# Kernel optimization log

Measured on AMD Instinct MI355X. Metric: run time of the kernel, lower is better.

Reference implementation:

```python
import jax, jax.numpy as jnp
import numpy as np

N = 100000        # nodes
E = 1600000       # edges (avg degree 16)
HID = 64          # hidden_dim
IN = 64           # input_dim
H = 4             # GAT heads
C = HID // H      # per-head channels (hidden//4)
LN_EPS = 1e-5
NEG_SLOPE = 0.2   # PyG GATConv default


def setup_inputs() -> dict:
    key = jax.random.key(0)
    ks = jax.random.split(key, 12)

    def nrm(k, shape, fan_in):
        return jax.random.normal(k, shape, jnp.float32) / np.sqrt(fan_in).astype(np.float32)

    x = jax.random.normal(ks[0], (N, IN), jnp.float32)
    edge_index = jax.random.randint(ks[1], (2, E), 0, N, jnp.int32)
    return {
        "x": x,
        "edge_index": edge_index,
        "emb_W": nrm(ks[2], (HID, IN), IN),
        "emb_b": jnp.zeros((HID,), jnp.float32),
        "e8_W": nrm(ks[3], (3, HID, HID), HID),
        "gat_W": nrm(ks[4], (3, HID, H * C), HID),
        "att_src": nrm(ks[5], (3, H, C), C),
        "att_dst": nrm(ks[6], (3, H, C), C),
        "gat_b": jnp.zeros((3, HID), jnp.float32),
        "fus_W": nrm(ks[7], (3, HID, 2 * HID), 2 * HID),
        "fus_b": jnp.zeros((3, HID), jnp.float32),
        "ln_g": jnp.ones((3, HID), jnp.float32),
        "ln_b": jnp.zeros((3, HID), jnp.float32),
        "r_W1": nrm(ks[8], (HID // 2, HID), HID),
        "r_b1": jnp.zeros((HID // 2,), jnp.float32),
        "r_W2": nrm(ks[9], (1, HID // 2), HID // 2),
        "r_b2": jnp.zeros((1,), jnp.float32),
    }


def _forward(x, edge_index, emb_W, emb_b, e8_W, gat_W, att_src, att_dst, gat_b,
             fus_W, fus_b, ln_g, ln_b, r_W1, r_b1, r_W2, r_b2):
    n = x.shape[0]
    row, col = edge_index[0], edge_index[1]

    # --- E8 symmetric normalization (depends only on graph; constant across layers) ---
    deg = jax.ops.segment_sum(jnp.ones_like(col, dtype=jnp.float32), col, num_segments=n)
    dinv = jnp.where(deg > 0, deg ** -0.5, 0.0)           # inf -> 0 as in torch code
    vals = dinv[row] * dinv[col]                           # [E]

    # --- GAT self-loops (PyG GATConv add_self_loops=True) ---
    loop = jnp.arange(n, dtype=row.dtype)
    src = jnp.concatenate([row, loop])                     # [E+N]
    dst = jnp.concatenate([col, loop])                     # [E+N]

    h = x @ emb_W.T + emb_b                                # embedding: [N, HID]

    for i in range(3):  # fixed 3 structurally-distinct blocks
        res = h
        # E8: sparse adj matmul then linear (no bias)
        x_e8 = jax.ops.segment_sum(vals[:, None] * h[col], row, num_segments=n) @ e8_W[i].T

        # GATConv (heads=4, concat)
        g = (h @ gat_W[i]).reshape(n, H, C)                # [N,H,C]
        a_s = (g * att_src[i]).sum(-1)                     # [N,H]
        a_d = (g * att_dst[i]).sum(-1)                     # [N,H]
        e = jax.nn.leaky_relu(a_s[src] + a_d[dst], NEG_SLOPE)   # [E+N,H]
        m = jax.lax.stop_gradient(jax.ops.segment_max(e, dst, num_segments=n))
        ee = jnp.exp(e - m[dst])
        s = jax.ops.segment_sum(ee, dst, num_segments=n)   # [N,H], >0 (self-loops)
        alpha = ee / s[dst]                                # per-dst softmax
        x_gat = jax.ops.segment_sum(alpha[:, :, None] * g[src], dst, num_segments=n)
        x_gat = x_gat.reshape(n, H * C) + gat_b[i]

        # fusion + residual + LayerNorm + ReLU (dropout is identity in eval)
        h = jnp.concatenate([x_e8, x_gat], axis=-1) @ fus_W[i].T + fus_b[i]
        h = h + res
        mu = h.mean(-1, keepdims=True)
        var = ((h - mu) ** 2).mean(-1, keepdims=True)
        h = (h - mu) * jax.lax.rsqrt(var + LN_EPS) * ln_g[i] + ln_b[i]
        h = jax.nn.relu(h)

    h1 = jax.nn.relu(h @ r_W1.T + r_b1)                    # [N, HID//2]
    return jax.nn.sigmoid(h1 @ r_W2.T + r_b2)              # [N, 1]


def reference(x, edge_index, emb_W, emb_b, e8_W, gat_W, att_src, att_dst, gat_b,
              fus_W, fus_b, ln_g, ln_b, r_W1, r_b1, r_W2, r_b2):
    return _forward(x, edge_index, emb_W, emb_b, e8_W, gat_W, att_src, att_dst, gat_b,
                    fus_W, fus_b, ln_g, ln_b, r_W1, r_b1, r_W2, r_b2)
```

## Files before the change

kernel.cpp:

```cpp
#include <hip/hip_runtime.h>
#include <hip/hip_bf16.h>
#include <hip/hip_fp16.h>

typedef __hip_bfloat16 bf16;
typedef unsigned short ushort_t;
typedef unsigned short us8 __attribute__((ext_vector_type(8)));
typedef _Float16 half8 __attribute__((ext_vector_type(8)));
typedef float f32x4 __attribute__((ext_vector_type(4)));

#define NEG 0.2f
#define LNEPS 1e-5f
#define BWD 512

__device__ __forceinline__ int plaus(unsigned int lo){
    lo &= 0x7FFFu;
    if (lo == 0) return 1;
    unsigned int ex = (lo >> 7) & 0xFF;
    return (ex >= 100 && ex <= 140) ? 1 : 0;
}

__device__ __forceinline__ float decode_slot(const ushort_t* s, long long i, int fl){
    long long base = i << fl;
    unsigned int hi = s[base + fl];
    unsigned int lo = s[base];
    unsigned int bits = (hi << 16) | (lo * (unsigned int)fl);
    return __uint_as_float(bits);
}

__device__ __forceinline__ unsigned encf(float f){
    int b = __float_as_int(f);
    return (b >= 0) ? ((unsigned)b | 0x80000000u) : (unsigned)(~b);
}
__device__ __forceinline__ float decf(unsigned k){
    return (k & 0x80000000u) ? __uint_as_float(k & 0x7FFFFFFFu)
                             : __uint_as_float(~k);
}

#define P_TOTAL 56577
#define CONV_BLKS 222
__global__ __launch_bounds__(256) void k_init(const void* p0, const void* p1, const void* p2,
        const void* p3, const void* p4, const void* p5, const void* p6, const void* p7,
        const void* p8, const void* p9, const void* p10, const void* p11, const void* p12,
        const void* p13, const void* p14, const void* xs,
        const int* __restrict__ row, const int* __restrict__ col, int E, int NBK,
        int* flags, float* P, int* bcnt, unsigned* mxsu){
    __shared__ int lh[512];
    int t = threadIdx.x;
    if (blockIdx.x >= CONV_BLKS){
        int hb = blockIdx.x - CONV_BLKS;
        for (int i = t; i < 2*NBK; i += 256) lh[i] = 0;
        __syncthreads();
        for (long long e = (long long)hb*256 + t; e < E; e += (long long)256*256){
            atomicAdd(&lh[row[e] >> 9], 1);
            atomicAdd(&lh[NBK + (col[e] >> 9)], 1);
        }
        __syncthreads();
        for (int i = t; i < 2*NBK; i += 256){
            int v = lh[i];
            if (v) atomicAdd(&bcnt[i], v);
        }
        return;
    }
    if (blockIdx.x == 0){
        if (t < 9){
            const void* dt[9] = {xs, p0, p2, p3, p4, p5, p7, p11, p13};
            const ushort_t* w = (const ushort_t*)dt[t];
            int all_bf = 1;
            for (int i = 0; i < 16; i++) all_bf &= plaus((unsigned int)w[i]);
            flags[t] = all_bf ? 0 : 1;
        } else if (t == 9){
            const ushort_t* w = (const ushort_t*)p9;
            flags[9] = (w[0] == 0x3F80u) ? 0 : 1;
        }
        if (t < 32) mxsu[t] = 0u;
    }
    int idx = blockIdx.x*256 + t;
    if (idx >= P_TOTAL) return;
    const int sizes[15] = {4096,64,12288,12288,192,192,192,24576,192,192,192,2048,32,32,1};
    const int fidx[15]  = {1,  -1,  2,    3,    4,  5,  -1, 6,    -1, 9,  -1, 7,   -1,8, -1};
    const void* ptrs[15] = {p0,p1,p2,p3,p4,p5,p6,p7,p8,p9,p10,p11,p12,p13,p14};
    int s = 0, base = 0;
    while (idx - base >= sizes[s]){ base += sizes[s]; s++; }
    int li = idx - base;
    int fi = fidx[s];
    int fl = 0;
    if (fi == 9){
        const ushort_t* w = (const ushort_t*)ptrs[s];
        fl = (w[0] == 0x3F80u) ? 0 : 1;
    } else if (fi >= 0){
        const ushort_t* w = (const ushort_t*)ptrs[s];
        int all_bf = 1;
        for (int i = 0; i < 16; i++) all_bf &= plaus((unsigned int)w[i]);
        fl = all_bf ? 0 : 1;
    }
    P[idx] = decode_slot((const ushort_t*)ptrs[s], li, fl);
}

#define PRW_B0 (3*8192)
#define PRW_B1 (PRW_B0 + 192)
#define PRW_B2 (PRW_B1 + 3*5120)
__global__ __launch_bounds__(256) void kb_scanprew(const int* __restrict__ bcnt,
        int* __restrict__ bptr_r, int* __restrict__ bptr_c,
        int* __restrict__ bcur_r, int* __restrict__ bcur_c, int NBK, int E,
        const float* __restrict__ fus_W, const float* __restrict__ e8_W,
        const float* __restrict__ gat_b, const float* __restrict__ fus_b,
        const float* __restrict__ gat_W, const float* __restrict__ att_src,
        const float* __restrict__ att_dst,
        _Float16* __restrict__ Bfrag, float* __restrict__ b2c, _Float16* __restrict__ Bg){
    __shared__ int sh[256];
    int t = threadIdx.x;
    if (blockIdx.x < 2){
        int side = blockIdx.x;
        const int* c = bcnt + side*NBK;
        int* bp = side ? bptr_c : bptr_r;
        int* bc = side ? bcur_c : bcur_r;
        int v = (t < NBK) ? c[t] : 0;
        sh[t] = v; __syncthreads();
        for (int off = 1; off < 256; off <<= 1){
            int add = (t >= off) ? sh[t-off] : 0;
// ... 179 lines not shown
            #pragma unroll
            for (int j = 0; j < 8; j++){
                A0[j] = (_Float16)__uint_as_float((unsigned)r0[j] << 16);
                A1[j] = (_Float16)__uint_as_float((unsigned)r1[j] << 16);
            }
        } else {
            const f32x4* xf = (const f32x4*)xs;
            f32x4 f0 = xf[(size_t)anode*16 + q*2];
            f32x4 f1 = xf[(size_t)anode*16 + q*2 + 1];
            f32x4 f2 = xf[(size_t)anode*16 + 8 + q*2];
            f32x4 f3 = xf[(size_t)anode*16 + 8 + q*2 + 1];
            #pragma unroll
            for (int j = 0; j < 4; j++){
                A0[j] = (_Float16)f0[j]; A0[4+j] = (_Float16)f1[j];
                A1[j] = (_Float16)f2[j]; A1[4+j] = (_Float16)f3[j];
            }
        }
        f32x4 acc[4];
        #pragma unroll
        for (int t = 0; t < 4; t++){
            f32x4 z = {0.f, 0.f, 0.f, 0.f};
            z = __builtin_amdgcn_mfma_f32_16x16x32_f16(A0, Be[t][0], z, 0, 0, 0);
            z = __builtin_amdgcn_mfma_f32_16x16x32_f16(A1, Be[t][1], z, 0, 0, 0);
            acc[t] = z;
        }
        #pragma unroll
        for (int r = 0; r < 4; r++){
            int node = nb + q*4 + r;
            int nd2 = q*4 + r;
            #pragma unroll
            for (int t = 0; t < 4; t++){
                float out = acc[t][r] + bj[t];
                int byte = nd2*128 + (t*16 + c)*2;
                byte ^= (nd2 & 7) << 4;
                *(_Float16*)((char*)tb + byte) = (_Float16)out;
                if (node < N){
                    h16[(size_t)node*64 + t*16 + c] = __float2half(out);
                    ht16[(size_t)node*64 + t*16 + c] = __float2half(dinv[node]*out);
                }
            }
        }
        int b0 = (c*128 + 16*q) ^ ((c & 7) << 4);
        int b1 = (c*128 + 64 + 16*q) ^ ((c & 7) << 4);
        half8 A0g = *(half8*)((char*)tb + b0);
        half8 A1g = *(half8*)((char*)tb + b1);
        f32x4 gacc[5];
        #pragma unroll
        for (int t = 0; t < 5; t++){
            f32x4 z = {0.f, 0.f, 0.f, 0.f};
            z = __builtin_amdgcn_mfma_f32_16x16x32_f16(A0g, Bg[t][0], z, 0, 0, 0);
            z = __builtin_amdgcn_mfma_f32_16x16x32_f16(A1g, Bg[t][1], z, 0, 0, 0);
            gacc[t] = z;
        }
        #pragma unroll
        for (int r = 0; r < 4; r++) lmax = fmaxf(lmax, gacc[4][r]);
        #pragma unroll
        for (int r = 0; r < 4; r++){
            int node = nb + q*4 + r;
            if (node < N){
                #pragma unroll
                for (int t = 0; t < 4; t++)
                    G16[(size_t)node*64 + t*16 + c] = __float2half(gacc[t][r]);
                if (c < 8){
                    int hx = c >> 1;
                    if (c & 1) a_d[node*4+hx] = gacc[4][r];
                    else       a_s[node*4+hx] = gacc[4][r];
                }
            }
        }
    }
    lmax = fmaxf(lmax, __shfl_xor(lmax, 16));
    lmax = fmaxf(lmax, __shfl_xor(lmax, 32));
    if (lane < 8) redm[wv][lane] = lmax;
    __syncthreads();
    if (threadIdx.x < 8){
        float m = fmaxf(fmaxf(redm[0][threadIdx.x], redm[1][threadIdx.x]),
                        fmaxf(redm[2][threadIdx.x], redm[3][threadIdx.x]));
        int hx = threadIdx.x >> 1;
        int ix = (threadIdx.x & 1) ? 4 + hx : hx;
        atomicMax((unsigned*)mxs + ix, encf(m));
    }
}

__device__ __forceinline__ float leaky(float t){ return t > 0.f ? t : NEG*t; }

__global__ __launch_bounds__(256) void k_gather(const __half* __restrict__ ht16,
        const __half* __restrict__ G16,
        const float* __restrict__ a_s, const float* __restrict__ a_d,
        const float* __restrict__ mxs, const float* __restrict__ dinv,
        const int* __restrict__ row_ptr, const int* __restrict__ re_col,
        const int* __restrict__ col_ptr, const int* __restrict__ ce_row,
        __half* __restrict__ Aj16, __half* __restrict__ xg16, int N){
    int lane = threadIdx.x & 63;
    int grp  = lane >> 3;
    int sub  = lane & 7;
    int hh   = sub >> 1;
    int wid  = (blockIdx.x*blockDim.x + threadIdx.x) >> 6;
    int v    = wid*8 + grp;
    if (v >= N) return;
    const us8* htb = (const us8*)ht16;
    const us8* gb  = (const us8*)G16;
    const unsigned* mu = (const unsigned*)mxs;
    float sh = leaky(decf(mu[hh]) + decf(mu[4+hh]));
    int rs = row_ptr[v], re = row_ptr[v+1];
    float a0[8] = {0,0,0,0,0,0,0,0}, a1[8] = {0,0,0,0,0,0,0,0};
    float a2[8] = {0,0,0,0,0,0,0,0}, a3[8] = {0,0,0,0,0,0,0,0};
    int i = rs;
    for (; i + 3 < re; i += 4){
        us8 q0 = htb[(size_t)re_col[i]*8 + sub];
        us8 q1 = htb[(size_t)re_col[i+1]*8 + sub];
        us8 q2 = htb[(size_t)re_col[i+2]*8 + sub];
        us8 q3 = htb[(size_t)re_col[i+3]*8 + sub];
        #pragma unroll
        for (int j = 0; j < 8; j++){
            a0[j] += __half2float(__ushort_as_half(q0[j]));
            a1[j] += __half2float(__ushort_as_half(q1[j]));
            a2[j] += __half2float(__ushort_as_half(q2[j]));
            a3[j] += __half2float(__ushort_as_half(q3[j]));
        }
    }
    for (; i < re; i++){
        us8 q0 = htb[(size_t)re_col[i]*8 + sub];
        #pragma unroll
        for (int j = 0; j < 8; j++) a0[j] += __half2float(__ushort_as_half(q0[j]));
    }
    float dv = dinv[v];
    us8 pa;
    #pragma unroll
    for (int j = 0; j < 8; j++)
        pa[j] = __half_as_ushort(__float2half(dv*((a0[j]+a1[j]) + (a2[j]+a3[j]))));
    ((us8*)Aj16)[(size_t)v*8 + sub] = pa;
    float adv = a_d[v*4+hh];
    float eesl = __expf(leaky(a_s[v*4+hh] + adv) - sh);
    float s0 = eesl, s1 = 0.f, s2 = 0.f, s3 = 0.f;
    {
        us8 g0 = gb[(size_t)v*8 + sub];
        #pragma unroll
        for (int j = 0; j < 8; j++){
            a0[j] = eesl * __half2float(__ushort_as_half(g0[j]));
            a1[j] = 0.f; a2[j] = 0.f; a3[j] = 0.f;
        }
    }
    int cs = col_ptr[v], ce = col_ptr[v+1];
    i = cs;
    for (; i + 3 < ce; i += 4){
        int r0 = ce_row[i], r1 = ce_row[i+1], r2 = ce_row[i+2], r3 = ce_row[i+3];
        float e0 = __expf(leaky(a_s[r0*4+hh] + adv) - sh);
        float e1 = __expf(leaky(a_s[r1*4+hh] + adv) - sh);
        float e2 = __expf(leaky(a_s[r2*4+hh] + adv) - sh);
        float e3 = __expf(leaky(a_s[r3*4+hh] + adv) - sh);
        us8 q0 = gb[(size_t)r0*8 + sub];
        us8 q1 = gb[(size_t)r1*8 + sub];
        us8 q2 = gb[(size_t)r2*8 + sub];
        us8 q3 = gb[(size_t)r3*8 + sub];
        #pragma unroll
        for (int j = 0; j < 8; j++){
            a0[j] += e0 * __half2float(__ushort_as_half(q0[j]));
            a1[j] += e1 * __half2float(__ushort_as_half(q1[j]));
            a2[j] += e2 * __half2float(__ushort_as_half(q2[j]));
            a3[j] += e3 * __half2float(__ushort_as_half(q3[j]));
        }
        s0 += e0; s1 += e1; s2 += e2; s3 += e3;
    }
    for (; i < ce; i++){
        int r0 = ce_row[i];
        float e0 = __expf(leaky(a_s[r0*4+hh] + adv) - sh);
        us8 q0 = gb[(size_t)r0*8 + sub];
        #pragma unroll
        for (int j = 0; j < 8; j++) a0[j] += e0 * __half2float(__ushort_as_half(q0[j]));
        s0 += e0;
    }
    float inv = 1.f/((s0+s1)+(s2+s3));
    us8 px;
    #pragma unroll
    for (int j = 0; j < 8; j++)
        px[j] = __half_as_ushort(__float2half(((a0[j]+a1[j]) + (a2[j]+a3[j]))*inv));
    ((us8*)xg16)[(size_t)v*8 + sub] = px;
}

__global__ __launch_bounds__(256) void k_fuse_g(
        const __half* __restrict__ Aj16, const __half* __restrict__ xg16,
        const float* __restrict__ dinv, __half* __restrict__ h16,
        __half* __restrict__ ht16,
        const _Float16* __restrict__ Bfrag, const float* __restrict__ b2c,
        const float* __restrict__ ln_g, const float* __restrict__ ln_b,
        const _Float16* __restrict__ Bgn, __half* __restrict__ G16,
        float* __restrict__ a_s, float* __restrict__ a_d,
        float* __restrict__ mxs_next, int N){
    __shared__ float redm[4][8];
    __shared__ _Float16 tbuf[4][1024];
    int lane = threadIdx.x & 63;
    int wv = threadIdx.x >> 6;
    int q = lane >> 4, c = lane & 15;
    _Float16* tb = tbuf[wv];
    half8 B[4][4];
    const half8* Bp = (const half8*)Bfrag;
    #pragma unroll
    for (int t = 0; t < 4; t++)
        #pragma unroll
        for (int kk = 0; kk < 4; kk++)
            B[t][kk] = Bp[(t*4+kk)*64 + lane];
    half8 Bg[5][2];
    const half8* Bgp = (const half8*)Bgn;
    #pragma unroll
    for (int t = 0; t < 5; t++)
        #pragma unroll
        for (int kk = 0; kk < 2; kk++)
            Bg[t][kk] = Bgp[(t*2+kk)*64 + lane];
    float bj[4], lg[4], lb[4];
    #pragma unroll
    for (int t = 0; t < 4; t++){
        int n = t*16 + c;
        bj[t] = b2c[n]; lg[t] = ln_g[n]; lb[t] = ln_b[n];
    }
    float lmax = -1e30f;
    int tiles = (N + 15) >> 4;
    int wid = (blockIdx.x*blockDim.x + threadIdx.x) >> 6;
    int nw  = (gridDim.x*blockDim.x) >> 6;
    for (int tile = wid; tile < tiles; tile += nw){
        int nb = tile << 4;
        int anode = nb + c; if (anode >= N) anode = N - 1;
        const half8* ap = (const half8*)(Aj16 + (size_t)anode*64);
        const half8* xp = (const half8*)(xg16 + (size_t)anode*64);
        half8 A0 = ap[q];
        half8 A1 = ap[4 + q];
        half8 A2 = xp[q];
        half8 A3 = xp[4 + q];
        f32x4 acc[4];
        #pragma unroll
        for (int t = 0; t < 4; t++){
            f32x4 z = {0.f, 0.f, 0.f, 0.f};
            z = __builtin_amdgcn_mfma_f32_16x16x32_f16(A0, B[t][0], z, 0, 0, 0);
            z = __builtin_amdgcn_mfma_f32_16x16x32_f16(A1, B[t][1], z, 0, 0, 0);
            z = __builtin_amdgcn_mfma_f32_16x16x32_f16(A2, B[t][2], z, 0, 0, 0);
            z = __builtin_amdgcn_mfma_f32_16x16x32_f16(A3, B[t][3], z, 0, 0, 0);
            acc[t] = z;
        }
        float y[4][4];
        #pragma unroll
        for (int r = 0; r < 4; r++){
            int node = nb + q*4 + r;
            int nd = node < N ? node : N - 1;
            #pragma unroll
            for (int t = 0; t < 4; t++)
                y[t][r] = acc[t][r] + bj[t]
                        + __half2float(h16[(size_t)nd*64 + t*16 + c]);
        }
        #pragma unroll
        for (int r = 0; r < 4; r++){
            int node = nb + q*4 + r;
            float s = (y[0][r] + y[1][r]) + (y[2][r] + y[3][r]);
            #pragma unroll
            for (int o = 1; o < 16; o <<= 1) s += __shfl_xor(s, o);
            float mu = s * (1.f/64.f);
            float d0 = y[0][r]-mu, d1 = y[1][r]-mu, d2 = y[2][r]-mu, d3 = y[3][r]-mu;
            float var = (d0*d0 + d1*d1) + (d2*d2 + d3*d3);
            #pragma unroll
            for (int o = 1; o < 16; o <<= 1) var += __shfl_xor(var, o);
            var *= (1.f/64.f);
            float rstd = rsqrtf(var + LNEPS);
            int nd2 = q*4 + r;
            #pragma unroll
            for (int t = 0; t < 4; t++){
                float out = (y[t][r]-mu)*rstd*lg[t] + lb[t];
                out = out > 0.f ? out : 0.f;
                int byte = nd2*128 + (t*16 + c)*2;
                byte ^= (nd2 & 7) << 4;
                *(_Float16*)((char*)tb + byte) = (_Float16)out;
                if (node < N){
                    h16[(size_t)node*64 + t*16 + c] = __float2half(out);
                    ht16[(size_t)node*64 + t*16 + c] = __float2half(dinv[node]*out);
                }
            }
        }
        int b0 = (c*128 + 16*q) ^ ((c & 7) << 4);
        int b1 = (c*128 + 64 + 16*q) ^ ((c & 7) << 4);
        half8 A0g = *(half8*)((char*)tb + b0);
        half8 A1g = *(half8*)((char*)tb + b1);
        f32x4 gacc[5];
        #pragma unroll
        for (int t = 0; t < 5; t++){
            f32x4 z = {0.f, 0.f, 0.f, 0.f};
            z = __builtin_amdgcn_mfma_f32_16x16x32_f16(A0g, Bg[t][0], z, 0, 0, 0);
            z = __builtin_amdgcn_mfma_f32_16x16x32_f16(A1g, Bg[t][1], z, 0, 0, 0);
            gacc[t] = z;
        }
        #pragma unroll
        for (int r = 0; r < 4; r++) lmax = fmaxf(lmax, gacc[4][r]);
        #pragma unroll
        for (int r = 0; r < 4; r++){
            int node = nb + q*4 + r;
            if (node < N){
                #pragma unroll
                for (int t = 0; t < 4; t++)
                    G16[(size_t)node*64 + t*16 + c] = __float2half(gacc[t][r]);
                if (c < 8){
                    int hx = c >> 1;
                    if (c & 1) a_d[node*4+hx] = gacc[4][r];
                    else       a_s[node*4+hx] = gacc[4][r];
                }
            }
        }
    }
    lmax = fmaxf(lmax, __shfl_xor(lmax, 16));
    lmax = fmaxf(lmax, __shfl_xor(lmax, 32));
    if (lane < 8) redm[wv][lane] = lmax;
    __syncthreads();
    if (threadIdx.x < 8){
        float m = fmaxf(fmaxf(redm[0][threadIdx.x], redm[1][threadIdx.x]),
                        fmaxf(redm[2][threadIdx.x], redm[3][threadIdx.x]));
        int hx = threadIdx.x >> 1;
        int ix = (threadIdx.x & 1) ? 4 + hx : hx;
        atomicMax((unsigned*)mxs_next + ix, encf(m));
    }
}

__global__ __launch_bounds__(256) void k_fuse_ro(
        const __half* __restrict__ Aj16, const __half* __restrict__ xg16,
        const __half* __restrict__ h16,
        const _Float16* __restrict__ Bfrag, const float* __restrict__ b2c,
        const float* __restrict__ ln_g, const float* __restrict__ ln_b,
        const float* __restrict__ rW1, const float* __restrict__ rb1,
        const float* __restrict__ rW2, const float* __restrict__ rb2,
        float* __restrict__ out, int N){
    __shared__ _Float16 tbuf[4][1024];
    int lane = threadIdx.x & 63;
    int wv = threadIdx.x >> 6;
    int q = lane >> 4, c = lane & 15;
    _Float16* tb = tbuf[wv];
    half8 B[4][4];
    const half8* Bp = (const half8*)Bfrag;
    #pragma unroll
    for (int t = 0; t < 4; t++)
        #pragma unroll
        for (int kk = 0; kk < 4; kk++)
            B[t][kk] = Bp[(t*4+kk)*64 + lane];
    half8 B1r[2][2];
    #pragma unroll
    for (int t = 0; t < 2; t++){
        #pragma unroll
        for (int kk = 0; kk < 2; kk++){
            half8 v;
            #pragma unroll
            for (int j = 0; j < 8; j++)
                v[j] = (_Float16)rW1[(t*16 + c)*64 + kk*32 + q*8 + j];
            B1r[t][kk] = v;
        }
    }
    float bj[4], lg[4], lb[4];
    #pragma unroll
    for (int t = 0; t < 4; t++){
        int n = t*16 + c;
        bj[t] = b2c[n]; lg[t] = ln_g[n]; lb[t] = ln_b[n];
    }
    float b1v[2] = {rb1[c], rb1[16 + c]};
    float w2a = rW2[c], w2b = rW2[16 + c];
    float b2v = rb2[0];
    int tiles = (N + 15) >> 4;
    int wid = (blockIdx.x*blockDim.x + threadIdx.x) >> 6;
    int nw  = (gridDim.x*blockDim.x) >> 6;
    for (int tile = wid; tile < tiles; tile += nw){
        int nb = tile << 4;
        int anode = nb + c; if (anode >= N) anode = N - 1;
        const half8* ap = (const half8*)(Aj16 + (size_t)anode*64);
        const half8* xp = (const half8*)(xg16 + (size_t)anode*64);
        half8 A0 = ap[q];
        half8 A1 = ap[4 + q];
        half8 A2 = xp[q];
        half8 A3 = xp[4 + q];
        f32x4 acc[4];
        #pragma unroll
        for (int t = 0; t < 4; t++){
            f32x4 z = {0.f, 0.f, 0.f, 0.f};
            z = __builtin_amdgcn_mfma_f32_16x16x32_f16(A0, B[t][0], z, 0, 0, 0);
            z = __builtin_amdgcn_mfma_f32_16x16x32_f16(A1, B[t][1], z, 0, 0, 0);
            z = __builtin_amdgcn_mfma_f32_16x16x32_f16(A2, B[t][2], z, 0, 0, 0);
            z = __builtin_amdgcn_mfma_f32_16x16x32_f16(A3, B[t][3], z, 0, 0, 0);
            acc[t] = z;
        }
        float y[4][4];
        #pragma unroll
        for (int r = 0; r < 4; r++){
            int node = nb + q*4 + r;
            int nd = node < N ? node : N - 1;
            #pragma unroll
            for (int t = 0; t < 4; t++)
                y[t][r] = acc[t][r] + bj[t]
                        + __half2float(h16[(size_t)nd*64 + t*16 + c]);
        }
        #pragma unroll
        for (int r = 0; r < 4; r++){
            float s = (y[0][r] + y[1][r]) + (y[2][r] + y[3][r]);
            #pragma unroll
            for (int o = 1; o < 16; o <<= 1) s += __shfl_xor(s, o);
            float mu = s * (1.f/64.f);
            float d0 = y[0][r]-mu, d1 = y[1][r]-mu, d2 = y[2][r]-mu, d3 = y[3][r]-mu;
            float var = (d0*d0 + d1*d1) + (d2*d2 + d3*d3);
            #pragma unroll
            for (int o = 1; o < 16; o <<= 1) var += __shfl_xor(var, o);
            var *= (1.f/64.f);
            float rstd = rsqrtf(var + LNEPS);
            int nd2 = q*4 + r;
            #pragma unroll
            for (int t = 0; t < 4; t++){
                float outv = (y[t][r]-mu)*rstd*lg[t] + lb[t];
                outv = outv > 0.f ? outv : 0.f;
                int byte = nd2*128 + (t*16 + c)*2;
                byte ^= (nd2 & 7) << 4;
                *(_Float16*)((char*)tb + byte) = (_Float16)outv;
            }
        }
        int b0 = (c*128 + 16*q) ^ ((c & 7) << 4);
        int b1 = (c*128 + 64 + 16*q) ^ ((c & 7) << 4);
        half8 A0g = *(half8*)((char*)tb + b0);
        half8 A1g = *(half8*)((char*)tb + b1);
        f32x4 racc[2];
        #pragma unroll
        for (int t = 0; t < 2; t++){
            f32x4 z = {0.f, 0.f, 0.f, 0.f};
            z = __builtin_amdgcn_mfma_f32_16x16x32_f16(A0g, B1r[t][0], z, 0, 0, 0);
            z = __builtin_amdgcn_mfma_f32_16x16x32_f16(A1g, B1r[t][1], z, 0, 0, 0);
            racc[t] = z;
        }
        #pragma unroll
        for (int r = 0; r < 4; r++){
            int node = nb + q*4 + r;
            float h1a = racc[0][r] + b1v[0]; h1a = h1a > 0.f ? h1a : 0.f;
            float h1b = racc[1][r] + b1v[1]; h1b = h1b > 0.f ? h1b : 0.f;
            float p = h1a*w2a + h1b*w2b;
            p += __shfl_xor(p, 1);
            p += __shfl_xor(p, 2);
            p += __shfl_xor(p, 4);
            p += __shfl_xor(p, 8);
            if (c == 0 && node < N){
                float z = p + b2v;
                out[node] = 1.f/(1.f + __expf(-z));
            }
        }
    }
}

extern "C" void kernel_launch(void* const* d_in, const int* in_sizes, int n_in,
                              void* d_out, int out_size, void* d_ws, size_t ws_size,
                              hipStream_t stream){
    const ushort_t* xs = (const ushort_t*)d_in[0];
    const int*      ei = (const int*)d_in[1];

    int N = in_sizes[0] / 64;
    int E = in_sizes[1] / 2;
    const int* row = ei;
    const int* col = ei + E;
    int NBK = (N + BWD - 1) / BWD;

    size_t mirF = (size_t)N*32;
    size_t stageF = (size_t)E;
    size_t aliasF = stageF > mirF ? stageF : mirF;

    float* f = (float*)d_ws;
    size_t o = 0;
    int*   flags = (int*)(f + o); o += 16;
    float* P     = f + o; o += P_TOTAL + 63;
    __half* h16  = (__half*)(f + o); o += mirF;
    __half* ht16 = (__half*)(f + o); o += mirF;
    __half* G16  = (__half*)(f + o); o += mirF;
    __half* Aj16 = (__half*)(f + o); size_t aoff = o; o += aliasF;
    __half* xg16 = (__half*)(f + o); size_t xoff = o; o += aliasF;
    unsigned* stage_r = (unsigned*)(f + aoff);
    unsigned* stage_c = (unsigned*)(f + xoff);
    float* a_s   = f + o; o += (size_t)N*4;
    float* a_d   = f + o; o += (size_t)N*4;
    float* mxs   = f + o; o += 32;
    float* dinv  = f + o; o += ((size_t)N + 15) & ~15ull;
    int* bcnt    = (int*)(f + o); o += 512;
    int* bptr_r  = (int*)(f + o); o += 512;
    int* bptr_c  = (int*)(f + o); o += 512;
    int* bcur_r  = (int*)(f + o); o += 512;
    int* bcur_c  = (int*)(f + o); o += 512;
    int* ptr_r   = (int*)(f + o); o += ((size_t)N + 16) & ~15ull;
    int* ptr_c   = (int*)(f + o); o += ((size_t)N + 16) & ~15ull;
    int* re_col  = (int*)(f + o); o += (size_t)E;
    int* ce_row  = (int*)(f + o); o += (size_t)E;
    float* b2c   = f + o; o += 3*64;
    _Float16* Bfrag = (_Float16*)(f + o); o += 3*4096;
    _Float16* Bg    = (_Float16*)(f + o); o += 3*2560;

    const float* emb_W   = P + 0;
    const float* emb_b   = P + 4096;
    const float* e8_W    = P + 4160;
    const float* gat_W   = P + 16448;
    const float* att_src = P + 28736;
    const float* att_dst = P + 28928;
    const float* gat_b   = P + 29120;
    const float* fus_W   = P + 29312;
    const float* fus_b   = P + 53888;
    const float* ln_g    = P + 54080;
    const float* ln_b    = P + 54272;
    const float* r_W1    = P + 54464;
    const float* r_b1    = P + 56512;
    const float* r_W2    = P + 56544;
    const float* r_b2    = P + 56576;

    hipMemsetAsync(bcnt, 0, 512*sizeof(int), stream);
    k_init<<<CONV_BLKS + 256, 256, 0, stream>>>(
        d_in[2],d_in[3],d_in[4],d_in[5],d_in[6],d_in[7],d_in[8],d_in[9],
        d_in[10],d_in[11],d_in[12],d_in[13],d_in[14],d_in[15],d_in[16],
        d_in[0], row, col, E, NBK, flags, P, bcnt, (unsigned*)mxs);

    int prwblk = (PRW_B2 + 255) / 256;
    kb_scanprew<<<2 + prwblk, 256, 0, stream>>>(bcnt, bptr_r, bptr_c, bcur_r, bcur_c,
                                                NBK, E, fus_W, e8_W, gat_b, fus_b,
                                                gat_W, att_src, att_dst, Bfrag, b2c, Bg);
    kb_bin<<<512, 1024, 0, stream>>>(row, col, bcur_r, bcur_c, stage_r, stage_c, NBK, E);
    kb_place<<<2*NBK, 1024, 0, stream>>>(stage_r, stage_c, bptr_r, bptr_c,
                                         ptr_r, ptr_c, re_col, ce_row, dinv, NBK, N, E);

    int tiles = (N + 15) / 16;
    int fgrid = (tiles + 7) / 8;
    int ggrid = (N + 31) / 32;
    k_embed_g<<<fgrid, 256, 0, stream>>>(xs, flags, emb_W, emb_b, dinv, Bg,
                                         h16, ht16, G16, a_s, a_d, mxs, N);
    for (int i = 0; i < 3; i++){
        k_gather<<<ggrid, 256, 0, stream>>>(ht16, G16, a_s, a_d, mxs + i*8, dinv,
                                            ptr_r, re_col, ptr_c, ce_row,
                                            Aj16, xg16, N);
        if (i < 2){
            k_fuse_g<<<fgrid, 256, 0, stream>>>(Aj16, xg16, dinv, h16, ht16,
                                                Bfrag + (size_t)i*8192, b2c + i*64,
                                                ln_g + i*64, ln_b + i*64,
                                                Bg + (size_t)(i+1)*5120, G16,
                                                a_s, a_d, mxs + (i+1)*8, N);
        } else {
            k_fuse_ro<<<fgrid, 256, 0, stream>>>(Aj16, xg16, h16,
                                                 Bfrag + (size_t)i*8192, b2c + i*64,
                                                 ln_g + i*64, ln_b + i*64,
                                                 r_W1, r_b1, r_W2, r_b2,
                                                 (float*)d_out, N);
        }
    }
}
```

Measured before the change: 635.8 us.

## Merge per-layer gather and fuse kernels into one persistent cooperative kernel

The six per-layer launches (gather, fuse, readout) are replaced by a single cooperative persistent kernel that loops over the three layers and uses grid-wide syncs between the gather and fuse phases. Weight fragments are now staged into shared memory per layer instead of being held in registers. This removes launch gaps and tail effects between the small kernels. In exchange it adds grid-sync overhead, caps the grid at occupancy-limited residency, and uses more LDS, which may reduce occupancy for the latency-bound gather phase.

```diff
diff --git a/kernel.cpp b/kernel.cpp
--- a/kernel.cpp
+++ b/kernel.cpp
@@ -1,6 +1,9 @@
 #include <hip/hip_runtime.h>
 #include <hip/hip_bf16.h>
 #include <hip/hip_fp16.h>
+#include <hip/hip_cooperative_groups.h>
+
+namespace cg = cooperative_groups;
 
 typedef __hip_bfloat16 bf16;
 typedef unsigned short ushort_t;
@@ -35,6 +38,8 @@
     return (k & 0x80000000u) ? __uint_as_float(k & 0x7FFFFFFFu)
                              : __uint_as_float(~k);
 }
+
+__device__ __forceinline__ float leaky(float t){ return t > 0.f ? t : NEG*t; }
 
 #define P_TOTAL 56577
 #define CONV_BLKS 222
@@ -380,361 +385,279 @@
     }
 }
 
-__device__ __forceinline__ float leaky(float t){ return t > 0.f ? t : NEG*t; }
-
-__global__ __launch_bounds__(256) void k_gather(const __half* __restrict__ ht16,
-        const __half* __restrict__ G16,
-        const float* __restrict__ a_s, const float* __restrict__ a_d,
-        const float* __restrict__ mxs, const float* __restrict__ dinv,
-        const int* __restrict__ row_ptr, const int* __restrict__ re_col,
-        const int* __restrict__ col_ptr, const int* __restrict__ ce_row,
-        __half* __restrict__ Aj16, __half* __restrict__ xg16, int N){
-    int lane = threadIdx.x & 63;
-    int grp  = lane >> 3;
-    int sub  = lane & 7;
-    int hh   = sub >> 1;
-    int wid  = (blockIdx.x*blockDim.x + threadIdx.x) >> 6;
-    int v    = wid*8 + grp;
-    if (v >= N) return;
+__global__ __launch_bounds__(256, 4) void k_layers(
+        __half* __restrict__ h16, __half* __restrict__ ht16, __half* __restrict__ G16,
+        float* __restrict__ a_s, float* __restrict__ a_d, float* __restrict__ mxs,
+        const float* __restrict__ dinv,
+        const int* __restrict__ ptr_r, const int* __restrict__ re_col,
+        const int* __restrict__ ptr_c, const int* __restrict__ ce_row,
+        const _Float16* __restrict__ BfragG, const float* __restrict__ b2cG,
+        const float* __restrict__ ln_gG, const float* __restrict__ ln_bG,
+        const _Float16* __restrict__ BgG,
+        const float* __restrict__ rW1, const float* __restrict__ rb1,
+        const float* __restrict__ rW2, const float* __restrict__ rb2,
+        __half* __restrict__ Aj16, __half* __restrict__ xg16,
+        float* __restrict__ out, int N){
+    cg::grid_group gridg = cg::this_grid();
+    __shared__ _Float16 Bsh[8192];
+    __shared__ _Float16 Bgsh[5120];
+    __shared__ _Float16 tbuf[4][1024];
+    __shared__ float redm[4][8];
+    int tid = threadIdx.x;
+    int lane = tid & 63, wv = tid >> 6;
+    int q = lane >> 4, c = lane & 15;
+    int grp = lane >> 3, sub = lane & 7, hh = sub >> 1;
+    _Float16* tb = tbuf[wv];
+    int wid0 = (blockIdx.x*256 + tid) >> 6;
+    int TW = (gridDim.x*256) >> 6;
+    const us8* gb  = (const us8*)G16;
     const us8* htb = (const us8*)ht16;
-    const us8* gb  = (const us8*)G16;
-    const unsigned* mu = (const unsigned*)mxs;
-    float sh = leaky(decf(mu[hh]) + decf(mu[4+hh]));
-    int rs = row_ptr[v], re = row_ptr[v+1];
-    float a0[8] = {0,0,0,0,0,0,0,0}, a1[8] = {0,0,0,0,0,0,0,0};
-    float a2[8] = {0,0,0,0,0,0,0,0}, a3[8] = {0,0,0,0,0,0,0,0};
-    int i = rs;
-    for (; i + 3 < re; i += 4){
-        us8 q0 = htb[(size_t)re_col[i]*8 + sub];
-        us8 q1 = htb[(size_t)re_col[i+1]*8 + sub];
-        us8 q2 = htb[(size_t)re_col[i+2]*8 + sub];
-        us8 q3 = htb[(size_t)re_col[i+3]*8 + sub];
-        #pragma unroll
-        for (int j = 0; j < 8; j++){
-            a0[j] += __half2float(__ushort_as_half(q0[j]));
-            a1[j] += __half2float(__ushort_as_half(q1[j]));
-            a2[j] += __half2float(__ushort_as_half(q2[j]));
-            a3[j] += __half2float(__ushort_as_half(q3[j]));
-        }
-    }
-    for (; i < re; i++){
-        us8 q0 = htb[(size_t)re_col[i]*8 + sub];
-        #pragma unroll
-        for (int j = 0; j < 8; j++) a0[j] += __half2float(__ushort_as_half(q0[j]));
-    }
-    float dv = dinv[v];
-    us8 pa;
-    #pragma unroll
-    for (int j = 0; j < 8; j++)
-        pa[j] = __half_as_ushort(__float2half(dv*((a0[j]+a1[j]) + (a2[j]+a3[j]))));
-    ((us8*)Aj16)[(size_t)v*8 + sub] = pa;
-    float adv = a_d[v*4+hh];
-    float eesl = __expf(leaky(a_s[v*4+hh] + adv) - sh);
-    float s0 = eesl, s1 = 0.f, s2 = 0.f, s3 = 0.f;
-    {
-        us8 g0 = gb[(size_t)v*8 + sub];
-        #pragma unroll
-        for (int j = 0; j < 8; j++){
-            a0[j] = eesl * __half2float(__ushort_as_half(g0[j]));
-            a1[j] = 0.f; a2[j] = 0.f; a3[j] = 0.f;
-        }
-    }
-    int cs = col_ptr[v], ce = col_ptr[v+1];
-    i = cs;
-    for (; i + 3 < ce; i += 4){
-        int r0 = ce_row[i], r1 = ce_row[i+1], r2 = ce_row[i+2], r3 = ce_row[i+3];
-        float e0 = __expf(leaky(a_s[r0*4+hh] + adv) - sh);
-        float e1 = __expf(leaky(a_s[r1*4+hh] + adv) - sh);
-        float e2 = __expf(leaky(a_s[r2*4+hh] + adv) - sh);
-        float e3 = __expf(leaky(a_s[r3*4+hh] + adv) - sh);
-        us8 q0 = gb[(size_t)r0*8 + sub];
-        us8 q1 = gb[(size_t)r1*8 + sub];
-        us8 q2 = gb[(size_t)r2*8 + sub];
-        us8 q3 = gb[(size_t)r3*8 + sub];
-        #pragma unroll
-        for (int j = 0; j < 8; j++){
-            a0[j] += e0 * __half2float(__ushort_as_half(q0[j]));
-            a1[j] += e1 * __half2float(__ushort_as_half(q1[j]));
-            a2[j] += e2 * __half2float(__ushort_as_half(q2[j]));
-            a3[j] += e3 * __half2float(__ushort_as_half(q3[j]));
-        }
-        s0 += e0; s1 += e1; s2 += e2; s3 += e3;
-    }
-    for (; i < ce; i++){
-        int r0 = ce_row[i];
-        float e0 = __expf(leaky(a_s[r0*4+hh] + adv) - sh);
-        us8 q0 = gb[(size_t)r0*8 + sub];
-        #pragma unroll
-        for (int j = 0; j < 8; j++) a0[j] += e0 * __half2float(__ushort_as_half(q0[j]));
-        s0 += e0;
-    }
-    float inv = 1.f/((s0+s1)+(s2+s3));
-    us8 px;
-    #pragma unroll
-    for (int j = 0; j < 8; j++)
-        px[j] = __half_as_ushort(__float2half(((a0[j]+a1[j]) + (a2[j]+a3[j]))*inv));
-    ((us8*)xg16)[(size_t)v*8 + sub] = px;
-}
-
-__global__ __launch_bounds__(256) void k_fuse_g(
-        const __half* __restrict__ Aj16, const __half* __restrict__ xg16,
-        const float* __restrict__ dinv, __half* __restrict__ h16,
-        __half* __restrict__ ht16,
-        const _Float16* __restrict__ Bfrag, const float* __restrict__ b2c,
-        const float* __restrict__ ln_g, const float* __restrict__ ln_b,
-        const _Float16* __restrict__ Bgn, __half* __restrict__ G16,
-        float* __restrict__ a_s, float* __restrict__ a_d,
-        float* __restrict__ mxs_next, int N){
-    __shared__ float redm[4][8];
-    __shared__ _Float16 tbuf[4][1024];
-    int lane = threadIdx.x & 63;
-    int wv = threadIdx.x >> 6;
-    int q = lane >> 4, c = lane & 15;
-    _Float16* tb = tbuf[wv];
-    half8 B[4][4];
-    const half8* Bp = (const half8*)Bfrag;
-    #pragma unroll
-    for (int t = 0; t < 4; t++)
-        #pragma unroll
-        for (int kk = 0; kk < 4; kk++)
-            B[t][kk] = Bp[(t*4+kk)*64 + lane];
-    half8 Bg[5][2];
-    const half8* Bgp = (const half8*)Bgn;
-    #pragma unroll
-    for (int t = 0; t < 5; t++)
-        #pragma unroll
-        for (int kk = 0; kk < 2; kk++)
-            Bg[t][kk] = Bgp[(t*2+kk)*64 + lane];
-    float bj[4], lg[4], lb[4];
-    #pragma unroll
-    for (int t = 0; t < 4; t++){
-        int n = t*16 + c;
-        bj[t] = b2c[n]; lg[t] = ln_g[n]; lb[t] = ln_b[n];
-    }
-    float lmax = -1e30f;
-    int tiles = (N + 15) >> 4;
-    int wid = (blockIdx.x*blockDim.x + threadIdx.x) >> 6;
-    int nw  = (gridDim.x*blockDim.x) >> 6;
-    for (int tile = wid; tile < tiles; tile += nw){
-        int nb = tile << 4;
-        int anode = nb + c; if (anode >= N) anode = N - 1;
-        const half8* ap = (const half8*)(Aj16 + (size_t)anode*64);
-        const half8* xp = (const half8*)(xg16 + (size_t)anode*64);
-        half8 A0 = ap[q];
-        half8 A1 = ap[4 + q];
-        half8 A2 = xp[q];
-        half8 A3 = xp[4 + q];
-        f32x4 acc[4];
+
+    for (int L = 0; L < 3; L++){
+        const unsigned* mup = (const unsigned*)mxs + L*8;
+        float shx = leaky(decf(mup[hh]) + decf(mup[4+hh]));
+        int NG = (N + 7) >> 3;
+        for (int w = wid0; w < NG; w += TW){
+            int v = w*8 + grp;
+            if (v < N){
+                int rs = ptr_r[v], re = ptr_r[v+1];
+                float a0[8] = {0,0,0,0,0,0,0,0}, a1[8] = {0,0,0,0,0,0,0,0};
+                float a2[8] = {0,0,0,0,0,0,0,0}, a3[8] = {0,0,0,0,0,0,0,0};
+                int i = rs;
+                for (; i + 3 < re; i += 4){
+                    us8 q0 = htb[(size_t)re_col[i]*8 + sub];
+                    us8 q1 = htb[(size_t)re_col[i+1]*8 + sub];
+                    us8 q2 = htb[(size_t)re_col[i+2]*8 + sub];
+                    us8 q3 = htb[(size_t)re_col[i+3]*8 + sub];
+                    #pragma unroll
+                    for (int j = 0; j < 8; j++){
+                        a0[j] += __half2float(__ushort_as_half(q0[j]));
+                        a1[j] += __half2float(__ushort_as_half(q1[j]));
+                        a2[j] += __half2float(__ushort_as_half(q2[j]));
+                        a3[j] += __half2float(__ushort_as_half(q3[j]));
+                    }
+                }
+                for (; i < re; i++){
+                    us8 q0 = htb[(size_t)re_col[i]*8 + sub];
+                    #pragma unroll
+                    for (int j = 0; j < 8; j++) a0[j] += __half2float(__ushort_as_half(q0[j]));
+                }
+                float dv = dinv[v];
+                us8 pa;
+                #pragma unroll
+                for (int j = 0; j < 8; j++)
+                    pa[j] = __half_as_ushort(__float2half(dv*((a0[j]+a1[j]) + (a2[j]+a3[j]))));
+                ((us8*)Aj16)[(size_t)v*8 + sub] = pa;
+                float adv = a_d[v*4+hh];
+                float eesl = __expf(leaky(a_s[v*4+hh] + adv) - shx);
+                float s0 = eesl, s1 = 0.f, s2 = 0.f, s3 = 0.f;
+                {
+                    us8 g0 = gb[(size_t)v*8 + sub];
+                    #pragma unroll
+                    for (int j = 0; j < 8; j++){
+                        a0[j] = eesl * __half2float(__ushort_as_half(g0[j]));
+                        a1[j] = 0.f; a2[j] = 0.f; a3[j] = 0.f;
+                    }
+                }
+                int cs = ptr_c[v], ce = ptr_c[v+1];
+                i = cs;
+                for (; i + 3 < ce; i += 4){
+                    int r0 = ce_row[i], r1 = ce_row[i+1], r2 = ce_row[i+2], r3 = ce_row[i+3];
+                    float e0 = __expf(leaky(a_s[r0*4+hh] + adv) - shx);
+                    float e1 = __expf(leaky(a_s[r1*4+hh] + adv) - shx);
+                    float e2 = __expf(leaky(a_s[r2*4+hh] + adv) - shx);
+                    float e3 = __expf(leaky(a_s[r3*4+hh] + adv) - shx);
+                    us8 q0 = gb[(size_t)r0*8 + sub];
+                    us8 q1 = gb[(size_t)r1*8 + sub];
+                    us8 q2 = gb[(size_t)r2*8 + sub];
+                    us8 q3 = gb[(size_t)r3*8 + sub];
+                    #pragma unroll
+                    for (int j = 0; j < 8; j++){
+                        a0[j] += e0 * __half2float(__ushort_as_half(q0[j]));
+                        a1[j] += e1 * __half2float(__ushort_as_half(q1[j]));
+                        a2[j] += e2 * __half2float(__ushort_as_half(q2[j]));
+                        a3[j] += e3 * __half2float(__ushort_as_half(q3[j]));
+                    }
+                    s0 += e0; s1 += e1; s2 += e2; s3 += e3;
+                }
+                for (; i < ce; i++){
+                    int r0 = ce_row[i];
+                    float e0 = __expf(leaky(a_s[r0*4+hh] + adv) - shx);
+                    us8 q0 = gb[(size_t)r0*8 + sub];
+                    #pragma unroll
+                    for (int j = 0; j < 8; j++) a0[j] += e0 * __half2float(__ushort_as_half(q0[j]));
+                    s0 += e0;
+                }
+                float inv = 1.f/((s0+s1)+(s2+s3));
+                us8 px;
+                #pragma unroll
+                for (int j = 0; j < 8; j++)
+                    px[j] = __half_as_ushort(__float2half(((a0[j]+a1[j]) + (a2[j]+a3[j]))*inv));
+                ((us8*)xg16)[(size_t)v*8 + sub] = px;
+            }
+        }
+        gridg.sync();
+
+        {
+            const half8* s = (const half8*)(BfragG + (size_t)L*8192);
+            half8* d = (half8*)Bsh;
+            for (int i = tid; i < 1024; i += 256) d[i] = s[i];
+        }
+        if (L < 2){
+            const half8* s = (const half8*)(BgG + (size_t)(L+1)*5120);
+            half8* d = (half8*)Bgsh;
+            for (int i = tid; i < 640; i += 256) d[i] = s[i];
+        } else {
+            for (int i = tid; i < 2048; i += 256){
+                int j = i & 7, ln = (i >> 3) & 63, kk = (i >> 9) & 1, tt = i >> 10;
+                int k = kk*32 + (ln >> 4)*8 + j;
+                int n = tt*16 + (ln & 15);
+                Bgsh[i] = (_Float16)rW1[n*64 + k];
+            }
+        }
+        __syncthreads();
+        const float* b2p = b2cG + L*64;
+        const float* lgp = ln_gG + L*64;
+        const float* lbp = ln_bG + L*64;
+        float bj[4], lg[4], lb[4];
         #pragma unroll
         for (int t = 0; t < 4; t++){
-            f32x4 z = {0.f, 0.f, 0.f, 0.f};
-            z = __builtin_amdgcn_mfma_f32_16x16x32_f16(A0, B[t][0], z, 0, 0, 0);
-            z = __builtin_amdgcn_mfma_f32_16x16x32_f16(A1, B[t][1], z, 0, 0, 0);
-            z = __builtin_amdgcn_mfma_f32_16x16x32_f16(A2, B[t][2], z, 0, 0, 0);
-            z = __builtin_amdgcn_mfma_f32_16x16x32_f16(A3, B[t][3], z, 0, 0, 0);
-            acc[t] = z;
-        }
-        float y[4][4];
-        #pragma unroll
-        for (int r = 0; r < 4; r++){
-            int node = nb + q*4 + r;
-            int nd = node < N ? node : N - 1;
-            #pragma unroll
-            for (int t = 0; t < 4; t++)
-                y[t][r] = acc[t][r] + bj[t]
-                        + __half2float(h16[(size_t)nd*64 + t*16 + c]);
-        }
-        #pragma unroll
-        for (int r = 0; r < 4; r++){
-            int node = nb + q*4 + r;
-            float s = (y[0][r] + y[1][r]) + (y[2][r] + y[3][r]);
-            #pragma unroll
-            for (int o = 1; o < 16; o <<= 1) s += __shfl_xor(s, o);
-            float mu = s * (1.f/64.f);
-            float d0 = y[0][r]-mu, d1 = y[1][r]-mu, d2 = y[2][r]-mu, d3 = y[3][r]-mu;
-            float var = (d0*d0 + d1*d1) + (d2*d2 + d3*d3);
-            #pragma unroll
-            for (int o = 1; o < 16; o <<= 1) var += __shfl_xor(var, o);
-            var *= (1.f/64.f);
-            float rstd = rsqrtf(var + LNEPS);
-            int nd2 = q*4 + r;
+            int n = t*16 + c;
+            bj[t] = b2p[n]; lg[t] = lgp[n]; lb[t] = lbp[n];
+        }
+        float b1v0 = 0.f, b1v1 = 0.f, w2a = 0.f, w2b = 0.f, b2v = 0.f;
+        if (L == 2){
+            b1v0 = rb1[c]; b1v1 = rb1[16 + c];
+            w2a = rW2[c];  w2b = rW2[16 + c];
+            b2v = rb2[0];
+        }
+        float lmax = -1e30f;
+        int tiles = (N + 15) >> 4;
+        for (int tile = wid0; tile < tiles; tile += TW){
+            int nb = tile << 4;
+            int anode = nb + c; if (anode >= N) anode = N - 1;
+            const half8* ap = (const half8*)(Aj16 + (size_t)anode*64);
+            const half8* xp = (const half8*)(xg16 + (size_t)anode*64);
+            half8 A0 = ap[q];
+            half8 A1 = ap[4 + q];
+            half8 A2 = xp[q];
+            half8 A3 = xp[4 + q];
+            f32x4 acc[4];
             #pragma unroll
             for (int t = 0; t < 4; t++){
-                float out = (y[t][r]-mu)*rstd*lg[t] + lb[t];
-                out = out > 0.f ? out : 0.f;
-                int byte = nd2*128 + (t*16 + c)*2;
-                byte ^= (nd2 & 7) << 4;
-                *(_Float16*)((char*)tb + byte) = (_Float16)out;
-                if (node < N){
-                    h16[(size_t)node*64 + t*16 + c] = __float2half(out);
-                    ht16[(size_t)node*64 + t*16 + c] = __float2half(dinv[node]*out);
-                }
-            }
-        }
-        int b0 = (c*128 + 16*q) ^ ((c & 7) << 4);
-        int b1 = (c*128 + 64 + 16*q) ^ ((c & 7) << 4);
-        half8 A0g = *(half8*)((char*)tb + b0);
-        half8 A1g = *(half8*)((char*)tb + b1);
-        f32x4 gacc[5];
-        #pragma unroll
-        for (int t = 0; t < 5; t++){
-            f32x4 z = {0.f, 0.f, 0.f, 0.f};
-            z = __builtin_amdgcn_mfma_f32_16x16x32_f16(A0g, Bg[t][0], z, 0, 0, 0);
-            z = __builtin_amdgcn_mfma_f32_16x16x32_f16(A1g, Bg[t][1], z, 0, 0, 0);
-            gacc[t] = z;
-        }
-        #pragma unroll
-        for (int r = 0; r < 4; r++) lmax = fmaxf(lmax, gacc[4][r]);
-        #pragma unroll
-        for (int r = 0; r < 4; r++){
-            int node = nb + q*4 + r;
-            if (node < N){
+                f32x4 z = {0.f, 0.f, 0.f, 0.f};
+                z = __builtin_amdgcn_mfma_f32_16x16x32_f16(A0, *(half8*)(Bsh + ((t*4+0)*64+lane)*8), z, 0, 0, 0);
+                z = __builtin_amdgcn_mfma_f32_16x16x32_f16(A1, *(half8*)(Bsh + ((t*4+1)*64+lane)*8), z, 0, 0, 0);
+                z = __builtin_amdgcn_mfma_f32_16x16x32_f16(A2, *(half8*)(Bsh + ((t*4+2)*64+lane)*8), z, 0, 0, 0);
+                z = __builtin_amdgcn_mfma_f32_16x16x32_f16(A3, *(half8*)(Bsh + ((t*4+3)*64+lane)*8), z, 0, 0, 0);
+                acc[t] = z;
+            }
+            float y[4][4];
+            #pragma unroll
+            for (int r = 0; r < 4; r++){
+                int node = nb + q*4 + r;
+                int nd = node < N ? node : N - 1;
                 #pragma unroll
                 for (int t = 0; t < 4; t++)
-                    G16[(size_t)node*64 + t*16 + c] = __float2half(gacc[t][r]);
-                if (c < 8){
-                    int hx = c >> 1;
-                    if (c & 1) a_d[node*4+hx] = gacc[4][r];
-                    else       a_s[node*4+hx] = gacc[4][r];
-                }
-            }
-        }
-    }
-    lmax = fmaxf(lmax, __shfl_xor(lmax, 16));
-    lmax = fmaxf(lmax, __shfl_xor(lmax, 32));
-    if (lane < 8) redm[wv][lane] = lmax;
-    __syncthreads();
-    if (threadIdx.x < 8){
-        float m = fmaxf(fmaxf(redm[0][threadIdx.x], redm[1][threadIdx.x]),
-                        fmaxf(redm[2][threadIdx.x], redm[3][threadIdx.x]));
-        int hx = threadIdx.x >> 1;
-        int ix = (threadIdx.x & 1) ? 4 + hx : hx;
-        atomicMax((unsigned*)mxs_next + ix, encf(m));
-    }
-}
-
-__global__ __launch_bounds__(256) void k_fuse_ro(
-        const __half* __restrict__ Aj16, const __half* __restrict__ xg16,
-        const __half* __restrict__ h16,
-        const _Float16* __restrict__ Bfrag, const float* __restrict__ b2c,
-        const float* __restrict__ ln_g, const float* __restrict__ ln_b,
-        const float* __restrict__ rW1, const float* __restrict__ rb1,
-        const float* __restrict__ rW2, const float* __restrict__ rb2,
-        float* __restrict__ out, int N){
-    __shared__ _Float16 tbuf[4][1024];
-    int lane = threadIdx.x & 63;
-    int wv = threadIdx.x >> 6;
-    int q = lane >> 4, c = lane & 15;
-    _Float16* tb = tbuf[wv];
-    half8 B[4][4];
-    const half8* Bp = (const half8*)Bfrag;
-    #pragma unroll
-    for (int t = 0; t < 4; t++)
-        #pragma unroll
-        for (int kk = 0; kk < 4; kk++)
-            B[t][kk] = Bp[(t*4+kk)*64 + lane];
-    half8 B1r[2][2];
-    #pragma unroll
-    for (int t = 0; t < 2; t++){
-        #pragma unroll
-        for (int kk = 0; kk < 2; kk++){
-            half8 v;
+                    y[t][r] = acc[t][r] + bj[t]
+                            + __half2float(h16[(size_t)nd*64 + t*16 + c]);
+            }
             #pragma unroll
-            for (int j = 0; j < 8; j++)
-                v[j] = (_Float16)rW1[(t*16 + c)*64 + kk*32 + q*8 + j];
-            B1r[t][kk] = v;
-        }
-    }
-    float bj[4], lg[4], lb[4];
-    #pragma unroll
-    for (int t = 0; t < 4; t++){
-        int n = t*16 + c;
-        bj[t] = b2c[n]; lg[t] = ln_g[n]; lb[t] = ln_b[n];
-    }
-    float b1v[2] = {rb1[c], rb1[16 + c]};
-    float w2a = rW2[c], w2b = rW2[16 + c];
-    float b2v = rb2[0];
-    int tiles = (N + 15) >> 4;
-    int wid = (blockIdx.x*blockDim.x + threadIdx.x) >> 6;
-    int nw  = (gridDim.x*blockDim.x) >> 6;
-    for (int tile = wid; tile < tiles; tile += nw){
-        int nb = tile << 4;
-        int anode = nb + c; if (anode >= N) anode = N - 1;
-        const half8* ap = (const half8*)(Aj16 + (size_t)anode*64);
-        const half8* xp = (const half8*)(xg16 + (size_t)anode*64);
-        half8 A0 = ap[q];
-        half8 A1 = ap[4 + q];
-        half8 A2 = xp[q];
-        half8 A3 = xp[4 + q];
-        f32x4 acc[4];
-        #pragma unroll
-        for (int t = 0; t < 4; t++){
-            f32x4 z = {0.f, 0.f, 0.f, 0.f};
-            z = __builtin_amdgcn_mfma_f32_16x16x32_f16(A0, B[t][0], z, 0, 0, 0);
-            z = __builtin_amdgcn_mfma_f32_16x16x32_f16(A1, B[t][1], z, 0, 0, 0);
-            z = __builtin_amdgcn_mfma_f32_16x16x32_f16(A2, B[t][2], z, 0, 0, 0);
-            z = __builtin_amdgcn_mfma_f32_16x16x32_f16(A3, B[t][3], z, 0, 0, 0);
-            acc[t] = z;
-        }
-        float y[4][4];
-        #pragma unroll
-        for (int r = 0; r < 4; r++){
-            int node = nb + q*4 + r;
-            int nd = node < N ? node : N - 1;
-            #pragma unroll
-            for (int t = 0; t < 4; t++)
-                y[t][r] = acc[t][r] + bj[t]
-                        + __half2float(h16[(size_t)nd*64 + t*16 + c]);
-        }
-        #pragma unroll
-        for (int r = 0; r < 4; r++){
-            float s = (y[0][r] + y[1][r]) + (y[2][r] + y[3][r]);
-            #pragma unroll
-            for (int o = 1; o < 16; o <<= 1) s += __shfl_xor(s, o);
-            float mu = s * (1.f/64.f);
-            float d0 = y[0][r]-mu, d1 = y[1][r]-mu, d2 = y[2][r]-mu, d3 = y[3][r]-mu;
-            float var = (d0*d0 + d1*d1) + (d2*d2 + d3*d3);
-            #pragma unroll
-            for (int o = 1; o < 16; o <<= 1) var += __shfl_xor(var, o);
-            var *= (1.f/64.f);
-            float rstd = rsqrtf(var + LNEPS);
-            int nd2 = q*4 + r;
-            #pragma unroll
-            for (int t = 0; t < 4; t++){
-                float outv = (y[t][r]-mu)*rstd*lg[t] + lb[t];
-                outv = outv > 0.f ? outv : 0.f;
-                int byte = nd2*128 + (t*16 + c)*2;
-                byte ^= (nd2 & 7) << 4;
-                *(_Float16*)((char*)tb + byte) = (_Float16)outv;
-            }
-        }
-        int b0 = (c*128 + 16*q) ^ ((c & 7) << 4);
-        int b1 = (c*128 + 64 + 16*q) ^ ((c & 7) << 4);
-        half8 A0g = *(half8*)((char*)tb + b0);
-        half8 A1g = *(half8*)((char*)tb + b1);
-        f32x4 racc[2];
-        #pragma unroll
-        for (int t = 0; t < 2; t++){
-            f32x4 z = {0.f, 0.f, 0.f, 0.f};
-            z = __builtin_amdgcn_mfma_f32_16x16x32_f16(A0g, B1r[t][0], z, 0, 0, 0);
-            z = __builtin_amdgcn_mfma_f32_16x16x32_f16(A1g, B1r[t][1], z, 0, 0, 0);
-            racc[t] = z;
-        }
-        #pragma unroll
-        for (int r = 0; r < 4; r++){
-            int node = nb + q*4 + r;
-            float h1a = racc[0][r] + b1v[0]; h1a = h1a > 0.f ? h1a : 0.f;
-            float h1b = racc[1][r] + b1v[1]; h1b = h1b > 0.f ? h1b : 0.f;
-            float p = h1a*w2a + h1b*w2b;
-            p += __shfl_xor(p, 1);
-            p += __shfl_xor(p, 2);
-            p += __shfl_xor(p, 4);
-            p += __shfl_xor(p, 8);
-            if (c == 0 && node < N){
-                float z = p + b2v;
-                out[node] = 1.f/(1.f + __expf(-z));
-            }
-        }
+            for (int r = 0; r < 4; r++){
+                int node = nb + q*4 + r;
+                float s = (y[0][r] + y[1][r]) + (y[2][r] + y[3][r]);
+                #pragma unroll
+                for (int o = 1; o < 16; o <<= 1) s += __shfl_xor(s, o);
+                float mu = s * (1.f/64.f);
+                float d0 = y[0][r]-mu, d1 = y[1][r]-mu, d2 = y[2][r]-mu, d3 = y[3][r]-mu;
+                float var = (d0*d0 + d1*d1) + (d2*d2 + d3*d3);
+                #pragma unroll
+                for (int o = 1; o < 16; o <<= 1) var += __shfl_xor(var, o);
+                var *= (1.f/64.f);
+                float rstd = rsqrtf(var + LNEPS);
+                int nd2 = q*4 + r;
+                #pragma unroll
+                for (int t = 0; t < 4; t++){
+                    float outv = (y[t][r]-mu)*rstd*lg[t] + lb[t];
+                    outv = outv > 0.f ? outv : 0.f;
+                    int byte = nd2*128 + (t*16 + c)*2;
+                    byte ^= (nd2 & 7) << 4;
+                    *(_Float16*)((char*)tb + byte) = (_Float16)outv;
+                    if (L < 2 && node < N){
+                        h16[(size_t)node*64 + t*16 + c] = __float2half(outv);
+                        ht16[(size_t)node*64 + t*16 + c] = __float2half(dinv[node]*outv);
+                    }
+                }
+            }
+            int bo0 = (c*128 + 16*q) ^ ((c & 7) << 4);
+            int bo1 = (c*128 + 64 + 16*q) ^ ((c & 7) << 4);
+            half8 A0g = *(half8*)((char*)tb + bo0);
+            half8 A1g = *(half8*)((char*)tb + bo1);
+            if (L < 2){
+                f32x4 gacc[5];
+                #pragma unroll
+                for (int t = 0; t < 5; t++){
+                    f32x4 z = {0.f, 0.f, 0.f, 0.f};
+                    z = __builtin_amdgcn_mfma_f32_16x16x32_f16(A0g, *(half8*)(Bgsh + ((t*2+0)*64+lane)*8), z, 0, 0, 0);
+                    z = __builtin_amdgcn_mfma_f32_16x16x32_f16(A1g, *(half8*)(Bgsh + ((t*2+1)*64+lane)*8), z, 0, 0, 0);
+                    gacc[t] = z;
+                }
+                #pragma unroll
+                for (int r = 0; r < 4; r++) lmax = fmaxf(lmax, gacc[4][r]);
+                #pragma unroll
+                for (int r = 0; r < 4; r++){
+                    int node = nb + q*4 + r;
+                    if (node < N){
+                        #pragma unroll
+                        for (int t = 0; t < 4; t++)
+                            G16[(size_t)node*64 + t*16 + c] = __float2half(gacc[t][r]);
+                        if (c < 8){
+                            int hx = c >> 1;
+                            if (c & 1) a_d[node*4+hx] = gacc[4][r];
+                            else       a_s[node*4+hx] = gacc[4][r];
+                        }
+                    }
+                }
+            } else {
+                f32x4 racc[2];
+                #pragma unroll
+                for (int t = 0; t < 2; t++){
+                    f32x4 z = {0.f, 0.f, 0.f, 0.f};
+                    z = __builtin_amdgcn_mfma_f32_16x16x32_f16(A0g, *(half8*)(Bgsh + ((t*2+0)*64+lane)*8), z, 0, 0, 0);
+                    z = __builtin_amdgcn_mfma_f32_16x16x32_f16(A1g, *(half8*)(Bgsh + ((t*2+1)*64+lane)*8), z, 0, 0, 0);
+                    racc[t] = z;
+                }
+                #pragma unroll
+                for (int r = 0; r < 4; r++){
+                    int node = nb + q*4 + r;
+                    float h1a = racc[0][r] + b1v0; h1a = h1a > 0.f ? h1a : 0.f;
+                    float h1b = racc[1][r] + b1v1; h1b = h1b > 0.f ? h1b : 0.f;
+                    float p = h1a*w2a + h1b*w2b;
+                    p += __shfl_xor(p, 1);
+                    p += __shfl_xor(p, 2);
+                    p += __shfl_xor(p, 4);
+                    p += __shfl_xor(p, 8);
+                    if (c == 0 && node < N){
+                        float z = p + b2v;
+                        out[node] = 1.f/(1.f + __expf(-z));
+                    }
+                }
+            }
+        }
+        if (L < 2){
+            lmax = fmaxf(lmax, __shfl_xor(lmax, 16));
+            lmax = fmaxf(lmax, __shfl_xor(lmax, 32));
+            if (lane < 8) redm[wv][lane] = lmax;
+            __syncthreads();
+            if (tid < 8){
+                float m = fmaxf(fmaxf(redm[0][tid], redm[1][tid]),
+                                fmaxf(redm[2][tid], redm[3][tid]));
+                int hx = tid >> 1;
+                int ix = (tid & 1) ? 4 + hx : hx;
+                atomicMax((unsigned*)mxs + (L+1)*8 + ix, encf(m));
+            }
+        }
+        gridg.sync();
     }
 }
 
@@ -814,25 +737,26 @@
 
     int tiles = (N + 15) / 16;
     int fgrid = (tiles + 7) / 8;
-    int ggrid = (N + 31) / 32;
     k_embed_g<<<fgrid, 256, 0, stream>>>(xs, flags, emb_W, emb_b, dinv, Bg,
                                          h16, ht16, G16, a_s, a_d, mxs, N);
-    for (int i = 0; i < 3; i++){
-        k_gather<<<ggrid, 256, 0, stream>>>(ht16, G16, a_s, a_d, mxs + i*8, dinv,
-                                            ptr_r, re_col, ptr_c, ce_row,
-                                            Aj16, xg16, N);
-        if (i < 2){
-            k_fuse_g<<<fgrid, 256, 0, stream>>>(Aj16, xg16, dinv, h16, ht16,
-                                                Bfrag + (size_t)i*8192, b2c + i*64,
-                                                ln_g + i*64, ln_b + i*64,
-                                                Bg + (size_t)(i+1)*5120, G16,
-                                                a_s, a_d, mxs + (i+1)*8, N);
-        } else {
-            k_fuse_ro<<<fgrid, 256, 0, stream>>>(Aj16, xg16, h16,
-                                                 Bfrag + (size_t)i*8192, b2c + i*64,
-                                                 ln_g + i*64, ln_b + i*64,
-                                                 r_W1, r_b1, r_W2, r_b2,
-                                                 (float*)d_out, N);
-        }
-    }
-}
+
+    static int coopGrid = 0;
+    if (coopGrid == 0){
+        int mb = 0;
+        hipOccupancyMaxActiveBlocksPerMultiprocessor(&mb, k_layers, 256, 0);
+        if (mb < 1) mb = 1;
+        hipDeviceProp_t prop;
+        hipGetDeviceProperties(&prop, 0);
+        coopGrid = mb * prop.multiProcessorCount;
+        if (coopGrid < 64) coopGrid = 64;
+    }
+    float* outP = (float*)d_out;
+    void* kargs[] = { (void*)&h16, (void*)&ht16, (void*)&G16,
+                      (void*)&a_s, (void*)&a_d, (void*)&mxs, (void*)&dinv,
+                      (void*)&ptr_r, (void*)&re_col, (void*)&ptr_c, (void*)&ce_row,
+                      (void*)&Bfrag, (void*)&b2c, (void*)&ln_g, (void*)&ln_b,
+                      (void*)&Bg, (void*)&r_W1, (void*)&r_b1, (void*)&r_W2, (void*)&r_b2,
+                      (void*)&Aj16, (void*)&xg16, (void*)&outP, (void*)&N };
+    hipLaunchCooperativeKernel((void*)k_layers, dim3(coopGrid), dim3(256),
+                               kargs, 0, stream);
+}
```

Measured after the change: 1.122 ms. +76.5%, slower.
